# Kernel optimization log

Hardware: AMD Instinct MI355X
Metric: run time of the kernel (lower is better)

Reference implementation:

```python
import jax, jax.numpy as jnp
import numpy as np

NUM_HEADS = 8
NUM_LEVELS = 4
NUM_POINTS = 4
EMBED = 256
HEAD_DIM = EMBED // NUM_HEADS
SPATIAL = [(100, 100), (50, 50), (25, 25), (13, 13)]  # (H, W) per level


def _bilinear_sample(val, grid):
    """torch.nn.functional.grid_sample(mode='bilinear', padding_mode='zeros', align_corners=False).
    val: [B, H, W, C], grid: [B, N, 2] with (x, y) in [-1, 1]. Returns [B, N, C]."""
    B, H, W, C = val.shape
    x = (grid[..., 0] + 1.0) * (W * 0.5) - 0.5
    y = (grid[..., 1] + 1.0) * (H * 0.5) - 0.5
    x0 = jnp.floor(x)
    y0 = jnp.floor(y)
    wx1 = x - x0
    wy1 = y - y0
    wx0 = 1.0 - wx1
    wy0 = 1.0 - wy1
    x0i = x0.astype(jnp.int32)
    y0i = y0.astype(jnp.int32)
    valf = val.reshape(B, H * W, C)

    def corner(xi, yi, w):
        valid = (xi >= 0) & (xi < W) & (yi >= 0) & (yi < H)
        idx = jnp.clip(yi, 0, H - 1) * W + jnp.clip(xi, 0, W - 1)
        v = jnp.take_along_axis(valf, idx[..., None], axis=1)  # [B, N, C]
        return v * (w * valid)[..., None]

    return (corner(x0i, y0i, wx0 * wy0) + corner(x0i + 1, y0i, wx1 * wy0)
            + corner(x0i, y0i + 1, wx0 * wy1) + corner(x0i + 1, y0i + 1, wx1 * wy1))


def setup_inputs() -> dict:
    key = jax.random.key(0)
    ks = jax.random.split(key, 12)
    bs, nq = 4, 6000
    nv = sum(h * w for h, w in SPATIAL)
    s = 0.02
    return {
        "query": jax.random.normal(ks[0], (bs, nq, EMBED), jnp.float32),
        "value": jax.random.normal(ks[1], (bs, nv, EMBED), jnp.float32),
        "reference_points": jax.random.uniform(ks[2], (bs, nq, NUM_LEVELS, 2), jnp.float32),
        "W_off": jax.random.normal(ks[3], (EMBED, NUM_HEADS * NUM_LEVELS * NUM_POINTS * 2), jnp.float32) * s,
        "b_off": jax.random.normal(ks[4], (NUM_HEADS * NUM_LEVELS * NUM_POINTS * 2,), jnp.float32),
        "W_attn": jax.random.normal(ks[5], (EMBED, NUM_HEADS * NUM_LEVELS * NUM_POINTS), jnp.float32) * s,
        "b_attn": jnp.zeros((NUM_HEADS * NUM_LEVELS * NUM_POINTS,), jnp.float32),
        "W_val": jax.random.normal(ks[6], (EMBED, EMBED), jnp.float32) * s,
        "b_val": jnp.zeros((EMBED,), jnp.float32),
        "W_out": jax.random.normal(ks[7], (EMBED, EMBED), jnp.float32) * s,
        "b_out": jnp.zeros((EMBED,), jnp.float32),
        "spatial_shapes": jnp.asarray(np.array(SPATIAL, dtype=np.int32)),
    }


def reference(query, value, reference_points, W_off, b_off, W_attn, b_attn,
              W_val, b_val, W_out, b_out, spatial_shapes):
    shapes = [(int(h), int(w)) for h, w in np.asarray(spatial_shapes)]
    bs, nq, _ = query.shape
    nv = value.shape[1]

    v = (value @ W_val + b_val).reshape(bs, nv, NUM_HEADS, HEAD_DIM)
    offsets = (query @ W_off + b_off).reshape(bs, nq, NUM_HEADS, NUM_LEVELS, NUM_POINTS, 2)
    aw = (query @ W_attn + b_attn).reshape(bs, nq, NUM_HEADS, NUM_LEVELS * NUM_POINTS)
    aw = jax.nn.softmax(aw, axis=-1).reshape(bs, nq, NUM_HEADS, NUM_LEVELS, NUM_POINTS)

    # offset normalizer is [W, H] per level
    norm = jnp.asarray([[w, h] for h, w in shapes], dtype=query.dtype)  # [L, 2]
    loc = reference_points[:, :, None, :, None, :] + offsets / norm[None, None, None, :, None, :]
    grids = 2.0 * loc - 1.0  # [bs, nq, H, L, P, 2]
    # -> [bs*H, nq*P, 2] per level
    grids = jnp.transpose(grids, (0, 2, 1, 3, 4, 5)).reshape(bs * NUM_HEADS, nq, NUM_LEVELS, NUM_POINTS, 2)

    v_bh = jnp.transpose(v, (0, 2, 1, 3)).reshape(bs * NUM_HEADS, nv, HEAD_DIM)
    sampled = []
    start = 0
    for l, (H_, W_) in enumerate(shapes):
        val_l = v_bh[:, start:start + H_ * W_].reshape(bs * NUM_HEADS, H_, W_, HEAD_DIM)
        grid_l = grids[:, :, l].reshape(bs * NUM_HEADS, nq * NUM_POINTS, 2)
        s_l = _bilinear_sample(val_l, grid_l).reshape(bs * NUM_HEADS, nq, NUM_POINTS, HEAD_DIM)
        sampled.append(s_l)
        start += H_ * W_
    sampled = jnp.stack(sampled, axis=2)  # [bs*H, nq, L, P, c]

    aw_bh = jnp.transpose(aw, (0, 2, 1, 3, 4)).reshape(bs * NUM_HEADS, nq, NUM_LEVELS, NUM_POINTS)
    out = (sampled * aw_bh[..., None]).sum(axis=(2, 3))  # [bs*H, nq, c]
    out = out.reshape(bs, NUM_HEADS, nq, HEAD_DIM).transpose(0, 2, 1, 3).reshape(bs, nq, EMBED)
    out = out @ W_out + b_out
    return out + query
```

## Files before the change

kernel.cpp:

```cpp
#include <hip/hip_runtime.h>
#include <hip/hip_bf16.h>

#define BS 4
#define NQ 6000
#define NV 13294
#define NH 8
#define HD 32
#define EMB 256
#define MV (BS * NV)
#define MQ (BS * NQ)

typedef __attribute__((ext_vector_type(8))) short short8;
typedef __attribute__((ext_vector_type(4))) float floatx4;
typedef __attribute__((ext_vector_type(2))) float floatx2;

__device__ __constant__ float LVL_DIM[4] = {100.f, 50.f, 25.f, 13.f};

__device__ inline unsigned short bf16bits(float f) {
  __hip_bfloat16 h = __float2bfloat16(f);
  return *reinterpret_cast<unsigned short*>(&h);
}
__device__ inline float bflo(unsigned int u) { return __uint_as_float(u << 16); }
__device__ inline float bfhi(unsigned int u) { return __uint_as_float(u & 0xffff0000u); }
__device__ inline floatx2 unpk(unsigned int u) {
  floatx2 r;
  r.x = __uint_as_float(u << 16);
  r.y = __uint_as_float(u & 0xffff0000u);
  return r;
}

#define LDS_STRIDE 40

__global__ __launch_bounds__(256) void wtrans_kernel(
    const float* __restrict__ W_val, const float* __restrict__ W_off,
    const float* __restrict__ W_attn, const float* __restrict__ W_out,
    unsigned short* __restrict__ Wt_val, unsigned short* __restrict__ Wt_qcat,
    unsigned short* __restrict__ Wt_out) {
  const int b = blockIdx.x, k = threadIdx.x;
  if (b < 256) {
    Wt_val[b * EMB + k] = bf16bits(W_val[k * 256 + b]);
  } else if (b < 640) {
    const int n = b - 256;
    float v = (n < 256) ? W_off[k * 256 + n] : W_attn[k * 128 + (n - 256)];
    Wt_qcat[n * EMB + k] = bf16bits(v);
  } else {
    const int n = b - 640;
    Wt_out[n * EMB + k] = bf16bits(W_out[k * 256 + n]);
  }
}

__device__ inline void loadA_f32(const float* __restrict__ A, int M, int m0,
                                 int k0, int tid, float4 ra[4]) {
  const int r = tid >> 1, half = tid & 1;
  const int row = m0 + r;
  if (row < M) {
    const float* src = A + (size_t)row * EMB + k0 + half * 16;
#pragma unroll
    for (int j = 0; j < 4; ++j) ra[j] = *(const float4*)(src + 4 * j);
  } else {
#pragma unroll
    for (int j = 0; j < 4; ++j) ra[j] = make_float4(0.f, 0.f, 0.f, 0.f);
  }
}
__device__ inline void storeA_lds(unsigned short* lds, int tid,
                                  const float4 ra[4]) {
  const int r = tid >> 1, half = tid & 1;
  unsigned short* dst = lds + r * LDS_STRIDE + half * 16;
#pragma unroll
  for (int j = 0; j < 4; ++j) {
    ushort4 u;
    u.x = bf16bits(ra[j].x);
    u.y = bf16bits(ra[j].y);
    u.z = bf16bits(ra[j].z);
    u.w = bf16bits(ra[j].w);
    *(ushort4*)(dst + 4 * j) = u;
  }
}
__device__ inline void loadB_bf16(const unsigned short* __restrict__ B, int M,
                                  int n0, int k0, int tid, uint4 rb[2]) {
  const int r = tid >> 1, half = tid & 1;
  const int row = n0 + r;
  if (row < M) {
    const unsigned short* src = B + (size_t)row * EMB + k0 + half * 16;
    rb[0] = *(const uint4*)(src);
    rb[1] = *(const uint4*)(src + 8);
  } else {
    rb[0] = rb[1] = make_uint4(0, 0, 0, 0);
  }
}
__device__ inline void storeB_lds(unsigned short* lds, int tid,
                                  const uint4 rb[2]) {
  const int r = tid >> 1, half = tid & 1;
  unsigned short* dst = lds + r * LDS_STRIDE + half * 16;
  *(uint4*)(dst) = rb[0];
  *(uint4*)(dst + 8) = rb[1];
}

__device__ inline void mfma_step(const unsigned short* ldsA,
                                 const unsigned short* ldsB, int wm, int wn,
                                 int lane, floatx4 acc[4][4]) {
  const unsigned short* ap =
      ldsA + (wm * 64 + (lane & 15)) * LDS_STRIDE + (lane >> 4) * 8;
  const unsigned short* bp =
      ldsB + (wn * 64 + (lane & 15)) * LDS_STRIDE + (lane >> 4) * 8;
  short8 af[4], bfr[4];
#pragma unroll
  for (int t = 0; t < 4; ++t) {
    af[t] = *(const short8*)(ap + t * 16 * LDS_STRIDE);
    bfr[t] = *(const short8*)(bp + t * 16 * LDS_STRIDE);
  }
#pragma unroll
  for (int mt = 0; mt < 4; ++mt)
#pragma unroll
    for (int nt = 0; nt < 4; ++nt)
      acc[mt][nt] = __builtin_amdgcn_mfma_f32_16x16x32_bf16(af[mt], bfr[nt],
                                                            acc[mt][nt], 0, 0, 0);
}

__device__ inline void gemm_loop_f32A(const float* __restrict__ A, int M,
                                      int m0, const unsigned short* __restrict__ B,
                                      int NB, int n0, unsigned short* ldsA,
                                      unsigned short* ldsB, int tid, int wm,
                                      int wn, int lane, floatx4 acc[4][4]) {
  float4 ra[4];
  uint4 rb[2];
  loadA_f32(A, M, m0, 0, tid, ra);
  loadB_bf16(B, NB, n0, 0, tid, rb);
#pragma unroll
  for (int k = 0; k < 8; ++k) {
    storeA_lds(ldsA, tid, ra);
    storeB_lds(ldsB, tid, rb);
    __syncthreads();
    if (k < 7) {
      loadA_f32(A, M, m0, (k + 1) * 32, tid, ra);
      loadB_bf16(B, NB, n0, (k + 1) * 32, tid, rb);
    }
    mfma_step(ldsA, ldsB, wm, wn, lane, acc);
    __syncthreads();
  }
}

__device__ inline void gemm_loop_bf16A(const unsigned short* __restrict__ A,
                                       int M, int m0,
                                       const unsigned short* __restrict__ B,
                                       int NB, int n0, unsigned short* ldsA,
                                       unsigned short* ldsB, int tid, int wm,
                                       int wn, int lane, floatx4 acc[4][4]) {
  uint4 ra[2], rb[2];
  loadB_bf16(A, M, m0, 0, tid, ra);
  loadB_bf16(B, NB, n0, 0, tid, rb);
#pragma unroll
  for (int k = 0; k < 8; ++k) {
    storeB_lds(ldsA, tid, ra);
    storeB_lds(ldsB, tid, rb);
    __syncthreads();
    if (k < 7) {
      loadB_bf16(A, M, m0, (k + 1) * 32, tid, ra);
      loadB_bf16(B, NB, n0, (k + 1) * 32, tid, rb);
    }
    mfma_step(ldsA, ldsB, wm, wn, lane, acc);
    __syncthreads();
  }
}

__global__ __launch_bounds__(256) void vqproj_kernel(
    const float* __restrict__ value, const unsigned short* __restrict__ Wt_val,
    const float* __restrict__ b_val, unsigned short* __restrict__ vbh,
    const float* __restrict__ query, const unsigned short* __restrict__ Wt_qcat,
    const float* __restrict__ refpts, const float* __restrict__ b_off,
    const float* __restrict__ b_attn, float* __restrict__ locbuf,
    float* __restrict__ awbuf) {
  __shared__ unsigned short ldsA[128 * LDS_STRIDE];
  __shared__ unsigned short ldsB[128 * LDS_STRIDE];
  const int tid = threadIdx.x, lane = tid & 63, w = tid >> 6;
  const int wm = w >> 1, wn = w & 1;
  floatx4 acc[4][4];
  const floatx4 zero = {0.f, 0.f, 0.f, 0.f};
#pragma unroll
  for (int i2 = 0; i2 < 4; i2++)
#pragma unroll
    for (int j = 0; j < 4; j++) acc[i2][j] = zero;
  const int quad = lane >> 4, cl = lane & 15;

  if (blockIdx.x < 832) {
    const int chunk = blockIdx.x >> 4, i = blockIdx.x & 15;
    const int m0 = (chunk * 8 + (i & 7)) * 128;
    const int n0 = (i >> 3) * 128;
    gemm_loop_f32A(value, MV, m0, Wt_val, 256, n0, ldsA, ldsB, tid, wm, wn,
                   lane, acc);
#pragma unroll
    for (int mt = 0; mt < 4; ++mt) {
#pragma unroll
      for (int r = 0; r < 4; ++r) {
        const int row = m0 + wm * 64 + mt * 16 + quad * 4 + r;
        if (row < MV) {
          const int b = row / NV, n = row - b * NV;
#pragma unroll
          for (int nt = 0; nt < 4; ++nt) {
            const int c = n0 + wn * 64 + nt * 16 + cl;
            const int h = c >> 5, d = c & 31;
            vbh[(((size_t)(b * NH + h)) * NV + n) * HD + d] =
                bf16bits(acc[mt][nt][r] + b_val[c]);
          }
        }
      }
    }
  } else {
    const int bid = blockIdx.x - 832;
    const int chunk = bid / 24, i = bid % 24;
    const int m_idx = chunk * 8 + (i & 7);
    if (m_idx >= 188) return;
    const int m0 = m_idx * 128;
    const int n0 = (i >> 3) * 128;
    gemm_loop_f32A(query, MQ, m0, Wt_qcat, 384, n0, ldsA, ldsB, tid, wm, wn,
                   lane, acc);
    if (n0 < 256) {
#pragma unroll
      for (int mt = 0; mt < 4; ++mt) {
#pragma unroll
        for (int r = 0; r < 4; ++r) {
          const int row = m0 + wm * 64 + mt * 16 + quad * 4 + r;
          if (row < MQ) {
#pragma unroll
            for (int nt = 0; nt < 4; ++nt) {
              const int c = n0 + wn * 64 + nt * 16 + cl;
              const int xy = c & 1, l = (c >> 3) & 3;
              const float dim = LVL_DIM[l];
              const float ref = refpts[(size_t)row * 8 + l * 2 + xy];
              locbuf[(size_t)row * 256 + c] =
                  ref * dim + acc[mt][nt][r] + b_off[c] - 0.5f;
            }
          }
        }
      }
    } else {
#pragma unroll
      for (int mt = 0; mt < 4; ++mt) {
#pragma unroll
        for (int r = 0; r < 4; ++r) {
          const int row = m0 + wm * 64 + mt * 16 + quad * 4 + r;
          if (row < MQ) {
#pragma unroll
            for (int nt = 0; nt < 4; ++nt) {
              const int ca = wn * 64 + nt * 16 + cl;
              float v = acc[mt][nt][r] + b_attn[ca];
              float m = v;
              m = fmaxf(m, __shfl_xor(m, 1));
              m = fmaxf(m, __shfl_xor(m, 2));
              m = fmaxf(m, __shfl_xor(m, 4));
              m = fmaxf(m, __shfl_xor(m, 8));
              float e = __expf(v - m);
              float s = e;
              s += __shfl_xor(s, 1);
              s += __shfl_xor(s, 2);
              s += __shfl_xor(s, 4);
              s += __shfl_xor(s, 8);
              awbuf[(size_t)row * 128 + ca] = e / s;
            }
          }
        }
      }
    }
  }
}

__global__ __launch_bounds__(256) void sample_kernel(
    const unsigned short* __restrict__ vbh, const float* __restrict__ locbuf,
    const float* __restrict__ awbuf, unsigned short* __restrict__ sampledb) {
  const int blk = blockIdx.x;
  const int t = blk >> 3;
  const int quarter = t / 1500;
  const int j = t - quarter * 1500;
  const int slice = (blk & 7) * 4 + quarter;
  const int h = slice & 7;
  const int w = threadIdx.x >> 6;
  const int lane = threadIdx.x & 63;
  const int row = (slice >> 3) * NQ + j * 4 + w;
  const int g = lane >> 2;
  const int d8 = lane & 3;
  const int l = g >> 2;

  const int W_ = (l < 2) ? ((l == 0) ? 100 : 50) : ((l == 2) ? 25 : 13);
  const int START = (l < 2) ? ((l == 0) ? 0 : 10000) : ((l == 2) ? 12500 : 13125);

  const float2 xy = *(const float2*)(locbuf + (size_t)row * 256 + h * 32 + g * 2);
  const float wgt = awbuf[(size_t)row * 128 + h * 16 + g];

  const float fx = floorf(xy.x), fy = floorf(xy.y);
  const int x0 = (int)fx, y0 = (int)fy;
  const float wx1 = xy.x - fx, wy1 = xy.y - fy;
  const float wx0 = 1.f - wx1, wy0 = 1.f - wy1;
  const int x0c = min(max(x0, 0), W_ - 1), x1c = min(max(x0 + 1, 0), W_ - 1);
  const int y0c = min(max(y0, 0), W_ - 1), y1c = min(max(y0 + 1, 0), W_ - 1);
  const float mx0 = ((unsigned)x0 < (unsigned)W_) ? wx0 : 0.f;
  const float mx1 = ((unsigned)(x0 + 1) < (unsigned)W_) ? wx1 : 0.f;
  const float my0 = ((unsigned)y0 < (unsigned)W_) ? wy0 : 0.f;
  const float my1 = ((unsigned)(y0 + 1) < (unsigned)W_) ? wy1 : 0.f;
  const float wy0w = wgt * my0, wy1w = wgt * my1;
  const float w00 = wy0w * mx0, w01 = wy0w * mx1;
  const float w10 = wy1w * mx0, w11 = wy1w * mx1;
  floatx2 w00v = {w00, w00}, w01v = {w01, w01};
  floatx2 w10v = {w10, w10}, w11v = {w11, w11};

  const unsigned int* base =
      (const unsigned int*)vbh + ((size_t)slice * NV + START) * 16 + d8 * 4;
  const int rb0 = y0c * W_, rb1 = y1c * W_;
  const uint4 u00 = *(const uint4*)(base + (size_t)(rb0 + x0c) * 16);
  const uint4 u01 = *(const uint4*)(base + (size_t)(rb0 + x1c) * 16);
  const uint4 u10 = *(const uint4*)(base + (size_t)(rb1 + x0c) * 16);
  const uint4 u11 = *(const uint4*)(base + (size_t)(rb1 + x1c) * 16);

  const unsigned int* p00 = &u00.x;
  const unsigned int* p01 = &u01.x;
  const unsigned int* p10 = &u10.x;
  const unsigned int* p11 = &u11.x;
  floatx2 a2[4];
#pragma unroll
  for (int k = 0; k < 4; ++k) {
    floatx2 s = w00v * unpk(p00[k]);
    s += w01v * unpk(p01[k]);
    s += w10v * unpk(p10[k]);
    s += w11v * unpk(p11[k]);
    a2[k] = s;
  }

  float a[8];
#pragma unroll
  for (int k = 0; k < 4; ++k) {
    a[2 * k] = a2[k].x;
    a[2 * k + 1] = a2[k].y;
  }
#pragma unroll
  for (int k = 0; k < 8; ++k) {
    a[k] += __shfl_xor(a[k], 4);
    a[k] += __shfl_xor(a[k], 8);
    a[k] += __shfl_xor(a[k], 16);
    a[k] += __shfl_xor(a[k], 32);
  }

  if (g == 0) {
    uint4 o;
    o.x = (unsigned)bf16bits(a[0]) | ((unsigned)bf16bits(a[1]) << 16);
    o.y = (unsigned)bf16bits(a[2]) | ((unsigned)bf16bits(a[3]) << 16);
    o.z = (unsigned)bf16bits(a[4]) | ((unsigned)bf16bits(a[5]) << 16);
    o.w = (unsigned)bf16bits(a[6]) | ((unsigned)bf16bits(a[7]) << 16);
    *(uint4*)(sampledb + (size_t)row * EMB + h * 32 + d8 * 8) = o;
  }
}

__global__ __launch_bounds__(256) void oproj_kernel(
    const unsigned short* __restrict__ sampledb,
    const unsigned short* __restrict__ Wt, const float* __restrict__ b_out,
    const float* __restrict__ query, float* __restrict__ out) {
  __shared__ unsigned short ldsA[128 * LDS_STRIDE];
  __shared__ unsigned short ldsB[128 * LDS_STRIDE];
  const int tid = threadIdx.x, lane = tid & 63, w = tid >> 6;
  const int wm = w >> 1, wn = w & 1;
  const int chunk = blockIdx.x >> 4, i = blockIdx.x & 15;
  const int m_idx = chunk * 8 + (i & 7);
  if (m_idx >= 188) return;
  const int m0 = m_idx * 128;
  const int n0 = (i >> 3) * 128;
  floatx4 acc[4][4];
  const floatx4 zero = {0.f, 0.f, 0.f, 0.f};
#pragma unroll
  for (int i2 = 0; i2 < 4; i2++)
#pragma unroll
    for (int j = 0; j < 4; j++) acc[i2][j] = zero;

  gemm_loop_bf16A(sampledb, MQ, m0, Wt, 256, n0, ldsA, ldsB, tid, wm, wn, lane,
                  acc);

  const int quad = lane >> 4, cl = lane & 15;
#pragma unroll
  for (int mt = 0; mt < 4; ++mt) {
#pragma unroll
    for (int r = 0; r < 4; ++r) {
      const int row = m0 + wm * 64 + mt * 16 + quad * 4 + r;
      if (row < MQ) {
#pragma unroll
        for (int nt = 0; nt < 4; ++nt) {
          const int c = n0 + wn * 64 + nt * 16 + cl;
          out[(size_t)row * EMB + c] =
              acc[mt][nt][r] + b_out[c] + query[(size_t)row * EMB + c];
        }
      }
    }
  }
}

extern "C" void kernel_launch(void* const* d_in, const int* in_sizes, int n_in,
                              void* d_out, int out_size, void* d_ws,
                              size_t ws_size, hipStream_t stream) {
  const float* query  = (const float*)d_in[0];
  const float* value  = (const float*)d_in[1];
  const float* refpts = (const float*)d_in[2];
  const float* W_off  = (const float*)d_in[3];
  const float* b_off  = (const float*)d_in[4];
  const float* W_attn = (const float*)d_in[5];
  const float* b_attn = (const float*)d_in[6];
  const float* W_val  = (const float*)d_in[7];
  const float* b_val  = (const float*)d_in[8];
  const float* W_out  = (const float*)d_in[9];
  const float* b_out  = (const float*)d_in[10];
  float* out = (float*)d_out;

  char* ws = (char*)d_ws;
  unsigned short* vbh = (unsigned short*)ws;
  float* locbuf = (float*)(ws + 27226112);
  float* awbuf = (float*)(ws + 51802112);
  unsigned short* sampledb = (unsigned short*)(ws + 64090112);
  unsigned short* Wt_val = (unsigned short*)(ws + 76378112);
  unsigned short* Wt_qcat = (unsigned short*)(ws + 76509184);
  unsigned short* Wt_out = (unsigned short*)(ws + 76705792);

  wtrans_kernel<<<896, 256, 0, stream>>>(W_val, W_off, W_attn, W_out, Wt_val,
                                         Wt_qcat, Wt_out);
  vqproj_kernel<<<1408, 256, 0, stream>>>(value, Wt_val, b_val, vbh, query,
                                          Wt_qcat, refpts, b_off, b_attn,
                                          locbuf, awbuf);
  sample_kernel<<<BS * NQ * NH / 4, 256, 0, stream>>>(vbh, locbuf, awbuf,
                                                      sampledb);
  oproj_kernel<<<384, 256, 0, stream>>>(sampledb, Wt_out, b_out, query, out);
}
```

Measured before the change: 258.8 us.

## Deepen GEMM K-tile to 64, process two rows per sample wave with transpose-reduce

The GEMM loops now stage 64-wide K slices in LDS, with stride 72, and issue two MFMA sub-steps per stage. This halves the number of barrier pairs per tile at the cost of more registers and LDS. The sample kernel now has each wave handle two query rows. Its cross-lane reduction is a butterfly transpose-reduce that spreads the dims across lanes, cutting the shuffle count, and each lane writes one bf16 scalar. Launch-bounds occupancy hints are added to the GEMM kernels and the sample kernel.

```diff
diff --git a/kernel.cpp b/kernel.cpp
--- a/kernel.cpp
+++ b/kernel.cpp
@@ -12,7 +12,6 @@
 
 typedef __attribute__((ext_vector_type(8))) short short8;
 typedef __attribute__((ext_vector_type(4))) float floatx4;
-typedef __attribute__((ext_vector_type(2))) float floatx2;
 
 __device__ __constant__ float LVL_DIM[4] = {100.f, 50.f, 25.f, 13.f};
 
@@ -22,14 +21,8 @@
 }
 __device__ inline float bflo(unsigned int u) { return __uint_as_float(u << 16); }
 __device__ inline float bfhi(unsigned int u) { return __uint_as_float(u & 0xffff0000u); }
-__device__ inline floatx2 unpk(unsigned int u) {
-  floatx2 r;
-  r.x = __uint_as_float(u << 16);
-  r.y = __uint_as_float(u & 0xffff0000u);
-  return r;
-}
-
-#define LDS_STRIDE 40
+
+#define LDSTR 72
 
 __global__ __launch_bounds__(256) void wtrans_kernel(
     const float* __restrict__ W_val, const float* __restrict__ W_off,
@@ -50,24 +43,24 @@
 }
 
 __device__ inline void loadA_f32(const float* __restrict__ A, int M, int m0,
-                                 int k0, int tid, float4 ra[4]) {
+                                 int k0, int tid, float4 ra[8]) {
   const int r = tid >> 1, half = tid & 1;
   const int row = m0 + r;
   if (row < M) {
-    const float* src = A + (size_t)row * EMB + k0 + half * 16;
-#pragma unroll
-    for (int j = 0; j < 4; ++j) ra[j] = *(const float4*)(src + 4 * j);
+    const float* src = A + (size_t)row * EMB + k0 + half * 32;
+#pragma unroll
+    for (int j = 0; j < 8; ++j) ra[j] = *(const float4*)(src + 4 * j);
   } else {
 #pragma unroll
-    for (int j = 0; j < 4; ++j) ra[j] = make_float4(0.f, 0.f, 0.f, 0.f);
+    for (int j = 0; j < 8; ++j) ra[j] = make_float4(0.f, 0.f, 0.f, 0.f);
   }
 }
 __device__ inline void storeA_lds(unsigned short* lds, int tid,
-                                  const float4 ra[4]) {
+                                  const float4 ra[8]) {
   const int r = tid >> 1, half = tid & 1;
-  unsigned short* dst = lds + r * LDS_STRIDE + half * 16;
-#pragma unroll
-  for (int j = 0; j < 4; ++j) {
+  unsigned short* dst = lds + r * LDSTR + half * 32;
+#pragma unroll
+  for (int j = 0; j < 8; ++j) {
     ushort4 u;
     u.x = bf16bits(ra[j].x);
     u.y = bf16bits(ra[j].y);
@@ -77,37 +70,38 @@
   }
 }
 __device__ inline void loadB_bf16(const unsigned short* __restrict__ B, int M,
-                                  int n0, int k0, int tid, uint4 rb[2]) {
+                                  int n0, int k0, int tid, uint4 rb[4]) {
   const int r = tid >> 1, half = tid & 1;
   const int row = n0 + r;
   if (row < M) {
-    const unsigned short* src = B + (size_t)row * EMB + k0 + half * 16;
-    rb[0] = *(const uint4*)(src);
-    rb[1] = *(const uint4*)(src + 8);
+    const unsigned short* src = B + (size_t)row * EMB + k0 + half * 32;
+#pragma unroll
+    for (int j = 0; j < 4; ++j) rb[j] = *(const uint4*)(src + 8 * j);
   } else {
-    rb[0] = rb[1] = make_uint4(0, 0, 0, 0);
+#pragma unroll
+    for (int j = 0; j < 4; ++j) rb[j] = make_uint4(0, 0, 0, 0);
   }
 }
 __device__ inline void storeB_lds(unsigned short* lds, int tid,
-                                  const uint4 rb[2]) {
+                                  const uint4 rb[4]) {
   const int r = tid >> 1, half = tid & 1;
-  unsigned short* dst = lds + r * LDS_STRIDE + half * 16;
-  *(uint4*)(dst) = rb[0];
-  *(uint4*)(dst + 8) = rb[1];
+  unsigned short* dst = lds + r * LDSTR + half * 32;
+#pragma unroll
+  for (int j = 0; j < 4; ++j) *(uint4*)(dst + 8 * j) = rb[j];
 }
 
 __device__ inline void mfma_step(const unsigned short* ldsA,
                                  const unsigned short* ldsB, int wm, int wn,
-                                 int lane, floatx4 acc[4][4]) {
+                                 int lane, int ksub, floatx4 acc[4][4]) {
   const unsigned short* ap =
-      ldsA + (wm * 64 + (lane & 15)) * LDS_STRIDE + (lane >> 4) * 8;
+      ldsA + (wm * 64 + (lane & 15)) * LDSTR + ksub + (lane >> 4) * 8;
   const unsigned short* bp =
-      ldsB + (wn * 64 + (lane & 15)) * LDS_STRIDE + (lane >> 4) * 8;
+      ldsB + (wn * 64 + (lane & 15)) * LDSTR + ksub + (lane >> 4) * 8;
   short8 af[4], bfr[4];
 #pragma unroll
   for (int t = 0; t < 4; ++t) {
-    af[t] = *(const short8*)(ap + t * 16 * LDS_STRIDE);
-    bfr[t] = *(const short8*)(bp + t * 16 * LDS_STRIDE);
+    af[t] = *(const short8*)(ap + t * 16 * LDSTR);
+    bfr[t] = *(const short8*)(bp + t * 16 * LDSTR);
   }
 #pragma unroll
   for (int mt = 0; mt < 4; ++mt)
@@ -122,20 +116,21 @@
                                       int NB, int n0, unsigned short* ldsA,
                                       unsigned short* ldsB, int tid, int wm,
                                       int wn, int lane, floatx4 acc[4][4]) {
-  float4 ra[4];
-  uint4 rb[2];
+  float4 ra[8];
+  uint4 rb[4];
   loadA_f32(A, M, m0, 0, tid, ra);
   loadB_bf16(B, NB, n0, 0, tid, rb);
 #pragma unroll
-  for (int k = 0; k < 8; ++k) {
+  for (int k = 0; k < 4; ++k) {
     storeA_lds(ldsA, tid, ra);
     storeB_lds(ldsB, tid, rb);
     __syncthreads();
-    if (k < 7) {
-      loadA_f32(A, M, m0, (k + 1) * 32, tid, ra);
-      loadB_bf16(B, NB, n0, (k + 1) * 32, tid, rb);
-    }
-    mfma_step(ldsA, ldsB, wm, wn, lane, acc);
+    if (k < 3) {
+      loadA_f32(A, M, m0, (k + 1) * 64, tid, ra);
+      loadB_bf16(B, NB, n0, (k + 1) * 64, tid, rb);
+    }
+    mfma_step(ldsA, ldsB, wm, wn, lane, 0, acc);
+    mfma_step(ldsA, ldsB, wm, wn, lane, 32, acc);
     __syncthreads();
   }
 }
@@ -146,32 +141,33 @@
                                        int NB, int n0, unsigned short* ldsA,
                                        unsigned short* ldsB, int tid, int wm,
                                        int wn, int lane, floatx4 acc[4][4]) {
-  uint4 ra[2], rb[2];
+  uint4 ra[4], rb[4];
   loadB_bf16(A, M, m0, 0, tid, ra);
   loadB_bf16(B, NB, n0, 0, tid, rb);
 #pragma unroll
-  for (int k = 0; k < 8; ++k) {
+  for (int k = 0; k < 4; ++k) {
     storeB_lds(ldsA, tid, ra);
     storeB_lds(ldsB, tid, rb);
     __syncthreads();
-    if (k < 7) {
-      loadB_bf16(A, M, m0, (k + 1) * 32, tid, ra);
-      loadB_bf16(B, NB, n0, (k + 1) * 32, tid, rb);
-    }
-    mfma_step(ldsA, ldsB, wm, wn, lane, acc);
+    if (k < 3) {
+      loadB_bf16(A, M, m0, (k + 1) * 64, tid, ra);
+      loadB_bf16(B, NB, n0, (k + 1) * 64, tid, rb);
+    }
+    mfma_step(ldsA, ldsB, wm, wn, lane, 0, acc);
+    mfma_step(ldsA, ldsB, wm, wn, lane, 32, acc);
     __syncthreads();
   }
 }
 
-__global__ __launch_bounds__(256) void vqproj_kernel(
+__global__ __launch_bounds__(256, 2) void vqproj_kernel(
     const float* __restrict__ value, const unsigned short* __restrict__ Wt_val,
     const float* __restrict__ b_val, unsigned short* __restrict__ vbh,
     const float* __restrict__ query, const unsigned short* __restrict__ Wt_qcat,
     const float* __restrict__ refpts, const float* __restrict__ b_off,
     const float* __restrict__ b_attn, float* __restrict__ locbuf,
     float* __restrict__ awbuf) {
-  __shared__ unsigned short ldsA[128 * LDS_STRIDE];
-  __shared__ unsigned short ldsB[128 * LDS_STRIDE];
+  __shared__ unsigned short ldsA[128 * LDSTR];
+  __shared__ unsigned short ldsB[128 * LDSTR];
   const int tid = threadIdx.x, lane = tid & 63, w = tid >> 6;
   const int wm = w >> 1, wn = w & 1;
   floatx4 acc[4][4];
@@ -264,96 +260,106 @@
   }
 }
 
-__global__ __launch_bounds__(256) void sample_kernel(
+__global__ __launch_bounds__(256, 4) void sample_kernel(
     const unsigned short* __restrict__ vbh, const float* __restrict__ locbuf,
     const float* __restrict__ awbuf, unsigned short* __restrict__ sampledb) {
   const int blk = blockIdx.x;
   const int t = blk >> 3;
-  const int quarter = t / 1500;
-  const int j = t - quarter * 1500;
+  const int quarter = t / 750;
+  const int j = t - quarter * 750;
   const int slice = (blk & 7) * 4 + quarter;
   const int h = slice & 7;
   const int w = threadIdx.x >> 6;
   const int lane = threadIdx.x & 63;
-  const int row = (slice >> 3) * NQ + j * 4 + w;
+  const int r0 = (slice >> 3) * NQ + j * 8 + w * 2;
   const int g = lane >> 2;
   const int d8 = lane & 3;
   const int l = g >> 2;
 
   const int W_ = (l < 2) ? ((l == 0) ? 100 : 50) : ((l == 2) ? 25 : 13);
   const int START = (l < 2) ? ((l == 0) ? 0 : 10000) : ((l == 2) ? 12500 : 13125);
-
-  const float2 xy = *(const float2*)(locbuf + (size_t)row * 256 + h * 32 + g * 2);
-  const float wgt = awbuf[(size_t)row * 128 + h * 16 + g];
-
-  const float fx = floorf(xy.x), fy = floorf(xy.y);
-  const int x0 = (int)fx, y0 = (int)fy;
-  const float wx1 = xy.x - fx, wy1 = xy.y - fy;
-  const float wx0 = 1.f - wx1, wy0 = 1.f - wy1;
-  const int x0c = min(max(x0, 0), W_ - 1), x1c = min(max(x0 + 1, 0), W_ - 1);
-  const int y0c = min(max(y0, 0), W_ - 1), y1c = min(max(y0 + 1, 0), W_ - 1);
-  const float mx0 = ((unsigned)x0 < (unsigned)W_) ? wx0 : 0.f;
-  const float mx1 = ((unsigned)(x0 + 1) < (unsigned)W_) ? wx1 : 0.f;
-  const float my0 = ((unsigned)y0 < (unsigned)W_) ? wy0 : 0.f;
-  const float my1 = ((unsigned)(y0 + 1) < (unsigned)W_) ? wy1 : 0.f;
-  const float wy0w = wgt * my0, wy1w = wgt * my1;
-  const float w00 = wy0w * mx0, w01 = wy0w * mx1;
-  const float w10 = wy1w * mx0, w11 = wy1w * mx1;
-  floatx2 w00v = {w00, w00}, w01v = {w01, w01};
-  floatx2 w10v = {w10, w10}, w11v = {w11, w11};
-
   const unsigned int* base =
       (const unsigned int*)vbh + ((size_t)slice * NV + START) * 16 + d8 * 4;
-  const int rb0 = y0c * W_, rb1 = y1c * W_;
-  const uint4 u00 = *(const uint4*)(base + (size_t)(rb0 + x0c) * 16);
-  const uint4 u01 = *(const uint4*)(base + (size_t)(rb0 + x1c) * 16);
-  const uint4 u10 = *(const uint4*)(base + (size_t)(rb1 + x0c) * 16);
-  const uint4 u11 = *(const uint4*)(base + (size_t)(rb1 + x1c) * 16);
-
-  const unsigned int* p00 = &u00.x;
-  const unsigned int* p01 = &u01.x;
-  const unsigned int* p10 = &u10.x;
-  const unsigned int* p11 = &u11.x;
-  floatx2 a2[4];
-#pragma unroll
-  for (int k = 0; k < 4; ++k) {
-    floatx2 s = w00v * unpk(p00[k]);
-    s += w01v * unpk(p01[k]);
-    s += w10v * unpk(p10[k]);
-    s += w11v * unpk(p11[k]);
-    a2[k] = s;
-  }
-
-  float a[8];
-#pragma unroll
-  for (int k = 0; k < 4; ++k) {
-    a[2 * k] = a2[k].x;
-    a[2 * k + 1] = a2[k].y;
-  }
-#pragma unroll
-  for (int k = 0; k < 8; ++k) {
-    a[k] += __shfl_xor(a[k], 4);
-    a[k] += __shfl_xor(a[k], 8);
-    a[k] += __shfl_xor(a[k], 16);
-    a[k] += __shfl_xor(a[k], 32);
-  }
-
-  if (g == 0) {
-    uint4 o;
-    o.x = (unsigned)bf16bits(a[0]) | ((unsigned)bf16bits(a[1]) << 16);
-    o.y = (unsigned)bf16bits(a[2]) | ((unsigned)bf16bits(a[3]) << 16);
-    o.z = (unsigned)bf16bits(a[4]) | ((unsigned)bf16bits(a[5]) << 16);
-    o.w = (unsigned)bf16bits(a[6]) | ((unsigned)bf16bits(a[7]) << 16);
-    *(uint4*)(sampledb + (size_t)row * EMB + h * 32 + d8 * 8) = o;
-  }
-}
-
-__global__ __launch_bounds__(256) void oproj_kernel(
+
+  float acc0[8], acc1[8];
+#pragma unroll
+  for (int rr = 0; rr < 2; ++rr) {
+    const int row = r0 + rr;
+    float* a = rr ? acc1 : acc0;
+    const float2 xy =
+        *(const float2*)(locbuf + (size_t)row * 256 + h * 32 + g * 2);
+    const float wgt = awbuf[(size_t)row * 128 + h * 16 + g];
+
+    const float fx = floorf(xy.x), fy = floorf(xy.y);
+    const int x0 = (int)fx, y0 = (int)fy;
+    const float wx1 = xy.x - fx, wy1 = xy.y - fy;
+    const float wx0 = 1.f - wx1, wy0 = 1.f - wy1;
+    const int x0c = min(max(x0, 0), W_ - 1), x1c = min(max(x0 + 1, 0), W_ - 1);
+    const int y0c = min(max(y0, 0), W_ - 1), y1c = min(max(y0 + 1, 0), W_ - 1);
+    const float mx0 = ((unsigned)x0 < (unsigned)W_) ? wx0 : 0.f;
+    const float mx1 = ((unsigned)(x0 + 1) < (unsigned)W_) ? wx1 : 0.f;
+    const float my0 = ((unsigned)y0 < (unsigned)W_) ? wy0 : 0.f;
+    const float my1 = ((unsigned)(y0 + 1) < (unsigned)W_) ? wy1 : 0.f;
+    const float wy0w = wgt * my0, wy1w = wgt * my1;
+    const float w00 = wy0w * mx0, w01 = wy0w * mx1;
+    const float w10 = wy1w * mx0, w11 = wy1w * mx1;
+
+    const int rb0 = y0c * W_, rb1 = y1c * W_;
+    const uint4 u00 = *(const uint4*)(base + (size_t)(rb0 + x0c) * 16);
+    const uint4 u01 = *(const uint4*)(base + (size_t)(rb0 + x1c) * 16);
+    const uint4 u10 = *(const uint4*)(base + (size_t)(rb1 + x0c) * 16);
+    const uint4 u11 = *(const uint4*)(base + (size_t)(rb1 + x1c) * 16);
+    const unsigned int* p00 = &u00.x;
+    const unsigned int* p01 = &u01.x;
+    const unsigned int* p10 = &u10.x;
+    const unsigned int* p11 = &u11.x;
+#pragma unroll
+    for (int k = 0; k < 4; ++k) {
+      a[2 * k] = w00 * bflo(p00[k]) + w01 * bflo(p01[k]) + w10 * bflo(p10[k]) +
+                 w11 * bflo(p11[k]);
+      a[2 * k + 1] = w00 * bfhi(p00[k]) + w01 * bfhi(p01[k]) +
+                     w10 * bfhi(p10[k]) + w11 * bfhi(p11[k]);
+    }
+  }
+
+  const bool b0 = (lane >> 2) & 1;
+  const bool b1 = (lane >> 3) & 1;
+  const bool b2 = (lane >> 4) & 1;
+#pragma unroll
+  for (int rr = 0; rr < 2; ++rr) {
+    float* v = rr ? acc1 : acc0;
+#pragma unroll
+    for (int jj = 0; jj < 4; ++jj) {
+      float lo = v[jj], hi = v[jj + 4];
+      float recv = __shfl_xor(b0 ? lo : hi, 4);
+      v[jj] = (b0 ? hi : lo) + recv;
+    }
+#pragma unroll
+    for (int jj = 0; jj < 2; ++jj) {
+      float lo = v[jj], hi = v[jj + 2];
+      float recv = __shfl_xor(b1 ? lo : hi, 8);
+      v[jj] = (b1 ? hi : lo) + recv;
+    }
+    {
+      float lo = v[0], hi = v[1];
+      float recv = __shfl_xor(b2 ? lo : hi, 16);
+      v[0] = (b2 ? hi : lo) + recv;
+    }
+    v[0] += __shfl_xor(v[0], 32);
+  }
+
+  const int dim = d8 * 8 + (b0 ? 4 : 0) + (b1 ? 2 : 0) + (b2 ? 1 : 0);
+  const int row = (lane < 32) ? r0 : (r0 + 1);
+  const float val = (lane < 32) ? acc0[0] : acc1[0];
+  sampledb[(size_t)row * EMB + h * 32 + dim] = bf16bits(val);
+}
+
+__global__ __launch_bounds__(256, 2) void oproj_kernel(
     const unsigned short* __restrict__ sampledb,
     const unsigned short* __restrict__ Wt, const float* __restrict__ b_out,
     const float* __restrict__ query, float* __restrict__ out) {
-  __shared__ unsigned short ldsA[128 * LDS_STRIDE];
-  __shared__ unsigned short ldsB[128 * LDS_STRIDE];
+  __shared__ unsigned short ldsA[128 * LDSTR];
+  __shared__ unsigned short ldsB[128 * LDSTR];
   const int tid = threadIdx.x, lane = tid & 63, w = tid >> 6;
   const int wm = w >> 1, wn = w & 1;
   const int chunk = blockIdx.x >> 4, i = blockIdx.x & 15;
@@ -419,7 +425,6 @@
   vqproj_kernel<<<1408, 256, 0, stream>>>(value, Wt_val, b_val, vbh, query,
                                           Wt_qcat, refpts, b_off, b_attn,
                                           locbuf, awbuf);
-  sample_kernel<<<BS * NQ * NH / 4, 256, 0, stream>>>(vbh, locbuf, awbuf,
-                                                      sampledb);
+  sample_kernel<<<24000, 256, 0, stream>>>(vbh, locbuf, awbuf, sampledb);
   oproj_kernel<<<384, 256, 0, stream>>>(sampledb, Wt_out, b_out, query, out);
 }
```

After: 247.7 us. 4.3% less time.
